# Kernel tuning notes

Measured on AMD Instinct MI355X. Metric: run time of the kernel, lower is better.

Reference implementation:

```python
import jax, jax.numpy as jnp
import numpy as np

N_ATOMS = 500000
MUL0, MUL1, MUL2 = 32, 16, 8      # geometry/output multiplicities for 0e,1o,2e
FMUL0, FMUL1 = 32, 16             # field multiplicities for 0e,1o

# real Wigner 3j for (1,1,2) in e3nn real basis order (l=1: y,z,x ; l=2: xy,yz,z2,zx,x2-y2)
# orthonormal symmetric-traceless basis matrices / sqrt(5) so that sum of squares == 1
def _w3j_112():
    s2 = 1.0 / np.sqrt(2.0); s6 = 1.0 / np.sqrt(6.0)
    C = np.zeros((3, 3, 5), np.float32)
    C[0, 2, 0] = C[2, 0, 0] = s2            # xy
    C[0, 1, 1] = C[1, 0, 1] = s2            # yz
    C[1, 1, 2] = 2.0 * s6; C[0, 0, 2] = -s6; C[2, 2, 2] = -s6  # z2
    C[1, 2, 3] = C[2, 1, 3] = s2            # zx
    C[2, 2, 4] = s2; C[0, 0, 4] = -s2       # x2-y2
    return C / np.sqrt(5.0)

W3J112 = jnp.asarray(_w3j_112())
INV_S3 = float(1.0 / np.sqrt(3.0))   # w3j(0,l,l) = I/sqrt(2l+1), w3j(1,1,0) = I/sqrt(3)
INV_S5 = float(1.0 / np.sqrt(5.0))   # w3j(2,0,2) = I/sqrt(5)
# e3nn FullyConnectedTensorProduct path coefficients (component irrep_normalization, element path_normalization):
# sqrt((2*l_out+1) / sum over paths with same output of mul1*mul2)
C0 = float(np.sqrt(1.0 / (MUL0 * FMUL0 + MUL1 * FMUL1)))          # -> 0e : 1/sqrt(1280)
C1 = float(np.sqrt(3.0 / (MUL0 * FMUL1 + MUL1 * FMUL0 + MUL2 * FMUL1)))  # -> 1o : sqrt(3/1152)
C2 = float(np.sqrt(5.0 / (MUL1 * FMUL1 + MUL2 * FMUL0)))          # -> 2e : sqrt(5/512)


def _forward(geometry_features, field_features,
             w_000, w_011, w_101, w_110, w_112, w_202, w_211,
             wl0, wl1, wl2):
    n = geometry_features.shape[0]
    g0 = geometry_features[:, :32]                       # (n, 32)
    g1 = geometry_features[:, 32:80].reshape(n, 16, 3)   # (n, 16, 3)
    g2 = geometry_features[:, 80:120].reshape(n, 8, 5)   # (n, 8, 5)
    f0 = field_features[:32]                             # (32,)  global, broadcast over atoms
    f1 = field_features[32:].reshape(16, 3)              # (16, 3)

    # --- tensor product paths (uvw connection mode) ---
    out0 = C0 * (jnp.einsum('uvw,zu,v->zw', w_000, g0, f0)
                 + INV_S3 * jnp.einsum('uvw,zui,vi->zw', w_110, g1, f1))
    out1 = C1 * (INV_S3 * jnp.einsum('uvw,zu,vk->zwk', w_011, g0, f1)
                 + INV_S3 * jnp.einsum('uvw,zuk,v->zwk', w_101, g1, f0)
                 + jnp.einsum('uvw,ijk,zuk,vi->zwj', w_211, W3J112, g2, f1))
    out2 = C2 * (jnp.einsum('uvw,ijk,zui,vj->zwk', w_112, W3J112, g1, f1)
                 + INV_S5 * jnp.einsum('uvw,zuk,v->zwk', w_202, g2, f0))

    # --- residual o3.Linear (matching irreps only, 1/sqrt(fan_in)) ---
    r0 = jnp.einsum('uw,zu->zw', wl0, g0) * float(1.0 / np.sqrt(MUL0))
    r1 = jnp.einsum('uw,zui->zwi', wl1, g1) * float(1.0 / np.sqrt(MUL1))
    r2 = jnp.einsum('uw,zui->zwi', wl2, g2) * float(1.0 / np.sqrt(MUL2))

    return jnp.concatenate([out0 + r0,
                            (out1 + r1).reshape(n, 48),
                            (out2 + r2).reshape(n, 40)], axis=1)


def setup_inputs() -> dict:
    key = jax.random.key(0)
    ks = jax.random.split(key, 12)
    rn = lambda k, s: jax.random.normal(k, s, dtype=jnp.float32)
    return {
        'geometry_features': rn(ks[0], (N_ATOMS, 120)),
        'field_features': rn(ks[1], (80,)),
        'w_000': rn(ks[2], (32, 32, 32)),  # (0e,0e)->0e
        'w_011': rn(ks[3], (32, 16, 16)),  # (0e,1o)->1o
        'w_101': rn(ks[4], (16, 32, 16)),  # (1o,0e)->1o
        'w_110': rn(ks[5], (16, 16, 32)),  # (1o,1o)->0e
        'w_112': rn(ks[6], (16, 16, 8)),   # (1o,1o)->2e
        'w_202': rn(ks[7], (8, 32, 8)),    # (2e,0e)->2e
        'w_211': rn(ks[8], (8, 16, 16)),   # (2e,1o)->1o
        'wl0': rn(ks[9], (32, 32)),
        'wl1': rn(ks[10], (16, 16)),
        'wl2': rn(ks[11], (8, 8)),
    }


def reference(geometry_features, field_features,
              w_000, w_011, w_101, w_110, w_112, w_202, w_211,
              wl0, wl1, wl2):
    return _forward(geometry_features, field_features,
                    w_000, w_011, w_101, w_110, w_112, w_202, w_211,
                    wl0, wl1, wl2)
```

## Files before the change

kernel.cpp:

```cpp
#include <hip/hip_runtime.h>

#define LDA 136
#define TM  64

__constant__ float W3J[45] = {
  0.f, 0.f, -0.18257418583505536f, 0.f, -0.31622776601683794f,
  0.f, 0.31622776601683794f, 0.f, 0.f, 0.f,
  0.31622776601683794f, 0.f, 0.f, 0.f, 0.f,
  0.f, 0.31622776601683794f, 0.f, 0.f, 0.f,
  0.f, 0.f, 0.36514837167011072f, 0.f, 0.f,
  0.f, 0.f, 0.f, 0.31622776601683794f, 0.f,
  0.31622776601683794f, 0.f, 0.f, 0.f, 0.f,
  0.f, 0.f, 0.f, 0.31622776601683794f, 0.f,
  0.f, 0.f, -0.18257418583505536f, 0.f, 0.31622776601683794f
};

__device__ __forceinline__ unsigned short f2bf(float f) {
  unsigned int u = __float_as_uint(f);
  u += 0x7FFFu + ((u >> 16) & 1u);
  return (unsigned short)(u >> 16);
}

__global__ void build_B_kernel(
    const float* __restrict__ field,
    const float* __restrict__ w000, const float* __restrict__ w011,
    const float* __restrict__ w101, const float* __restrict__ w110,
    const float* __restrict__ w112, const float* __restrict__ w202,
    const float* __restrict__ w211, const float* __restrict__ wl0,
    const float* __restrict__ wl1,  const float* __restrict__ wl2,
    unsigned short* __restrict__ Bt)
{
  const float C0  = 0.02795084971874737f;
  const float C1  = 0.051031036307982884f;
  const float C2  = 0.09882117688026186f;
  const float IS3 = 0.57735026918962576f;
  const float IS5 = 0.44721359549995794f;

  int n = blockIdx.x;
  int k = threadIdx.x;
  float val = 0.0f;

  if (n < 120 && k < 120) {
    if (n < 32) {
      int w = n;
      if (k < 32) {
        int u = k;
        float a = 0.f;
        for (int v = 0; v < 32; ++v) a += w000[u*1024 + v*32 + w] * field[v];
        val = C0 * a + wl0[u*32 + w] * 0.17677669529663689f;
      } else if (k < 80) {
        int u = (k-32)/3, i = (k-32)%3;
        float a = 0.f;
        for (int v = 0; v < 16; ++v) a += w110[u*512 + v*32 + w] * field[32 + v*3 + i];
        val = C0 * IS3 * a;
      }
    } else if (n < 80) {
      int w = (n-32)/3, j = (n-32)%3;
      if (k < 32) {
        int u = k;
        float a = 0.f;
        for (int v = 0; v < 16; ++v) a += w011[u*256 + v*16 + w] * field[32 + v*3 + j];
        val = C1 * IS3 * a;
      } else if (k < 80) {
        int u = (k-32)/3, i = (k-32)%3;
        if (i == j) {
          float a = 0.f;
          for (int v = 0; v < 32; ++v) a += w101[u*512 + v*16 + w] * field[v];
          val = C1 * IS3 * a + wl1[u*16 + w] * 0.25f;
        }
      } else {
        int u = (k-80)/5, kk = (k-80)%5;
        float c0w = W3J[0*15 + j*5 + kk];
        float c1w = W3J[1*15 + j*5 + kk];
        float c2w = W3J[2*15 + j*5 + kk];
        float a = 0.f;
        for (int v = 0; v < 16; ++v) {
          float s = c0w*field[32+v*3+0] + c1w*field[32+v*3+1] + c2w*field[32+v*3+2];
          a += w211[u*256 + v*16 + w] * s;
        }
        val = C1 * a;
      }
    } else {
      int w = (n-80)/5, k2 = (n-80)%5;
      if (k >= 32 && k < 80) {
        int u = (k-32)/3, i = (k-32)%3;
        float c0w = W3J[i*15 + 0*5 + k2];
        float c1w = W3J[i*15 + 1*5 + k2];
        float c2w = W3J[i*15 + 2*5 + k2];
        float a = 0.f;
        for (int v = 0; v < 16; ++v) {
          float s = c0w*field[32+v*3+0] + c1w*field[32+v*3+1] + c2w*field[32+v*3+2];
          a += w112[u*128 + v*8 + w] * s;
        }
        val = C2 * a;
      } else if (k >= 80) {
        int u = (k-80)/5, kk = (k-80)%5;
        if (kk == k2) {
          float a = 0.f;
          for (int v = 0; v < 32; ++v) a += w202[u*256 + v*8 + w] * field[v];
          val = C2 * IS5 * a + wl2[u*8 + w] * 0.35355339059327378f;
        }
      }
    }
  }
  Bt[n*128 + k] = f2bf(val);
}

typedef __attribute__((ext_vector_type(8))) __bf16 bf16x8;
typedef __attribute__((ext_vector_type(4))) float  f32x4;

__global__ __launch_bounds__(256) void coupling_main(
    const float* __restrict__ geom, const unsigned short* __restrict__ Btg,
    float* __restrict__ out, int natoms)
{
  __shared__ alignas(16) unsigned short Alds[TM  * LDA];
  __shared__ alignas(16) unsigned short Blds[128 * LDA];

  int tid = threadIdx.x;
  long long base = (long long)blockIdx.x * TM;

  #pragma unroll
  for (int r = 0; r < 8; ++r) {
    int g   = tid + r * 256;
    int row = g >> 4;
    int col = (g & 15) * 8;
    uint4 v = ((const uint4*)Btg)[g];
    *((uint4*)&Blds[row * LDA + col]) = v;
  }
  if (tid < TM) {
    *((uint4*)&Alds[tid * LDA + 120]) = make_uint4(0u, 0u, 0u, 0u);
  }
  #pragma unroll
  for (int r = 0; r < 4; ++r) {
    int g = tid + r * 256;
    if (g < 960) {
      int row = g / 15;
      int col = (g - row * 15) * 8;
      long long atom = base + row;
      uint4 pk;
      if (atom < natoms) {
        const float* src = geom + (long long)atom * 120 + col;
        float4 fa = ((const float4*)src)[0];
        float4 fb = ((const float4*)src)[1];
        pk.x = ((unsigned)f2bf(fa.y) << 16) | f2bf(fa.x);
        pk.y = ((unsigned)f2bf(fa.w) << 16) | f2bf(fa.z);
        pk.z = ((unsigned)f2bf(fb.y) << 16) | f2bf(fb.x);
        pk.w = ((unsigned)f2bf(fb.w) << 16) | f2bf(fb.z);
      } else {
        pk = make_uint4(0u, 0u, 0u, 0u);
      }
      *((uint4*)&Alds[row * LDA + col]) = pk;
    }
  }
  __syncthreads();

  int lane = tid & 63;
  int wave = tid >> 6;
  int mrow = lane & 15;
  int kq   = lane >> 4;

  f32x4 zero = {0.f, 0.f, 0.f, 0.f};
  f32x4 acc[8];
  #pragma unroll
  for (int t = 0; t < 8; ++t) acc[t] = zero;

  const unsigned short* arow = &Alds[(wave * 16 + mrow) * LDA + kq * 8];
  const unsigned short* brow = &Blds[mrow * LDA + kq * 8];

  #pragma unroll
  for (int ks = 0; ks < 4; ++ks) {
    bf16x8 af = __builtin_bit_cast(bf16x8, *(const uint4*)(arow + ks * 32));
    #pragma unroll
    for (int t = 0; t < 8; ++t) {
      bf16x8 bf_ = __builtin_bit_cast(bf16x8, *(const uint4*)(brow + t * 16 * LDA + ks * 32));
      acc[t] = __builtin_amdgcn_mfma_f32_16x16x32_bf16(af, bf_, acc[t], 0, 0, 0);
    }
  }

  long long atom0 = base + wave * 16 + kq * 4;
  #pragma unroll
  for (int t = 0; t < 8; ++t) {
    int n = t * 16 + mrow;
    if (n < 120) {
      #pragma unroll
      for (int r2 = 0; r2 < 4; ++r2) {
        long long atom = atom0 + r2;
        if (atom < natoms) out[atom * 120 + n] = acc[t][r2];
      }
    }
  }
}

extern "C" void kernel_launch(void* const* d_in, const int* in_sizes, int n_in,
                              void* d_out, int out_size, void* d_ws, size_t ws_size,
                              hipStream_t stream) {
  const float* geom  = (const float*)d_in[0];
  const float* field = (const float*)d_in[1];
  const float* w000  = (const float*)d_in[2];
  const float* w011  = (const float*)d_in[3];
  const float* w101  = (const float*)d_in[4];
  const float* w110  = (const float*)d_in[5];
  const float* w112  = (const float*)d_in[6];
  const float* w202  = (const float*)d_in[7];
  const float* w211  = (const float*)d_in[8];
  const float* wl0   = (const float*)d_in[9];
  const float* wl1   = (const float*)d_in[10];
  const float* wl2   = (const float*)d_in[11];
  float* out = (float*)d_out;
  unsigned short* Bt = (unsigned short*)d_ws;

  int natoms = in_sizes[0] / 120;

  build_B_kernel<<<dim3(128), dim3(128), 0, stream>>>(
      field, w000, w011, w101, w110, w112, w202, w211, wl0, wl1, wl2, Bt);

  int ntiles = (natoms + TM - 1) / TM;
  coupling_main<<<dim3(ntiles), dim3(256), 0, stream>>>(geom, Bt, out, natoms);
}
```

Measured before the change: 421.7 us.

## Stage output tile through LDS for coalesced nontemporal stores; read B from global

The B matrix is no longer copied into shared memory. Each MFMA now loads its B fragments straight from global memory, where they are expected to hit in cache. The accumulator tile is written to a shared buffer that reuses the A tile's space, then stored to global memory as contiguous float4 rows with nontemporal stores instead of scattered 4-byte writes. This is meant to cut uncoalesced store traffic and shrink the LDS footprint so occupancy can rise. The cost is two extra barriers and B reads going through the cache rather than LDS.

```diff
diff --git a/kernel.cpp b/kernel.cpp
--- a/kernel.cpp
+++ b/kernel.cpp
@@ -2,6 +2,7 @@
 
 #define LDA 136
 #define TM  64
+#define CST 132
 
 __constant__ float W3J[45] = {
   0.f, 0.f, -0.18257418583505536f, 0.f, -0.31622776601683794f,
@@ -113,23 +114,13 @@
     const float* __restrict__ geom, const unsigned short* __restrict__ Btg,
     float* __restrict__ out, int natoms)
 {
-  __shared__ alignas(16) unsigned short Alds[TM  * LDA];
-  __shared__ alignas(16) unsigned short Blds[128 * LDA];
+  __shared__ alignas(16) unsigned char smem[TM * CST * 4];
+  unsigned short* Al = (unsigned short*)smem;
+  float*          Cl = (float*)smem;
 
   int tid = threadIdx.x;
   long long base = (long long)blockIdx.x * TM;
 
-  #pragma unroll
-  for (int r = 0; r < 8; ++r) {
-    int g   = tid + r * 256;
-    int row = g >> 4;
-    int col = (g & 15) * 8;
-    uint4 v = ((const uint4*)Btg)[g];
-    *((uint4*)&Blds[row * LDA + col]) = v;
-  }
-  if (tid < TM) {
-    *((uint4*)&Alds[tid * LDA + 120]) = make_uint4(0u, 0u, 0u, 0u);
-  }
   #pragma unroll
   for (int r = 0; r < 4; ++r) {
     int g = tid + r * 256;
@@ -149,8 +140,11 @@
       } else {
         pk = make_uint4(0u, 0u, 0u, 0u);
       }
-      *((uint4*)&Alds[row * LDA + col]) = pk;
-    }
+      *((uint4*)&Al[row * LDA + col]) = pk;
+    }
+  }
+  if (tid < TM) {
+    *((uint4*)&Al[tid * LDA + 120]) = make_uint4(0u, 0u, 0u, 0u);
   }
   __syncthreads();
 
@@ -164,28 +158,42 @@
   #pragma unroll
   for (int t = 0; t < 8; ++t) acc[t] = zero;
 
-  const unsigned short* arow = &Alds[(wave * 16 + mrow) * LDA + kq * 8];
-  const unsigned short* brow = &Blds[mrow * LDA + kq * 8];
+  const unsigned short* arow = &Al[(wave * 16 + mrow) * LDA + kq * 8];
+  const uint4* Bq = ((const uint4*)Btg) + mrow * 16 + kq;
 
   #pragma unroll
   for (int ks = 0; ks < 4; ++ks) {
     bf16x8 af = __builtin_bit_cast(bf16x8, *(const uint4*)(arow + ks * 32));
     #pragma unroll
     for (int t = 0; t < 8; ++t) {
-      bf16x8 bf_ = __builtin_bit_cast(bf16x8, *(const uint4*)(brow + t * 16 * LDA + ks * 32));
+      bf16x8 bf_ = __builtin_bit_cast(bf16x8, Bq[t * 256 + ks * 4]);
       acc[t] = __builtin_amdgcn_mfma_f32_16x16x32_bf16(af, bf_, acc[t], 0, 0, 0);
     }
   }
 
-  long long atom0 = base + wave * 16 + kq * 4;
+  __syncthreads();
+
+  int crow = wave * 16 + kq * 4;
   #pragma unroll
   for (int t = 0; t < 8; ++t) {
     int n = t * 16 + mrow;
-    if (n < 120) {
-      #pragma unroll
-      for (int r2 = 0; r2 < 4; ++r2) {
-        long long atom = atom0 + r2;
-        if (atom < natoms) out[atom * 120 + n] = acc[t][r2];
+    #pragma unroll
+    for (int r2 = 0; r2 < 4; ++r2) {
+      Cl[(crow + r2) * CST + n] = acc[t][r2];
+    }
+  }
+  __syncthreads();
+
+  #pragma unroll
+  for (int r = 0; r < 8; ++r) {
+    int g = tid + r * 256;
+    if (g < 1920) {
+      int row = g / 30;
+      int c4  = g - row * 30;
+      long long atom = base + row;
+      if (atom < natoms) {
+        f32x4 v = *(const f32x4*)&Cl[row * CST + c4 * 4];
+        __builtin_nontemporal_store(v, (f32x4*)(out + atom * 120 + c4 * 4));
       }
     }
   }
```

Result: slower. 489.2 us (+16.0%).

## Use persistent blocks with register double-buffered prefetch of geometry tiles

Applied to the files above, without the earlier changes.

Launches a capped persistent grid where each block loads the B matrix into LDS once and loops over atom tiles. Geometry rows are loaded straight into registers two tiles ahead, converted to bf16 and fed to MFMA without LDS staging for A. This aims to hide global load latency and remove repeated B loads and per-block sync overhead, at the cost of more registers and less block-level parallelism.

```diff
diff --git a/kernel.cpp b/kernel.cpp
--- a/kernel.cpp
+++ b/kernel.cpp
@@ -109,15 +109,82 @@
 typedef __attribute__((ext_vector_type(8))) __bf16 bf16x8;
 typedef __attribute__((ext_vector_type(4))) float  f32x4;
 
-__global__ __launch_bounds__(256) void coupling_main(
+#define PREFETCH(TT, LO, HI) do {                                        \
+    if ((TT) < ntiles) {                                                 \
+      long long atom_ = (long long)(TT) * TM + rowin;                    \
+      const float* ga_ = geom + atom_ * 120 + kq * 8;                    \
+      bool full_ = ((long long)(TT) * TM + TM) <= (long long)natoms;     \
+      bool ina_  = full_ || (atom_ < natoms);                            \
+      _Pragma("unroll")                                                  \
+      for (int ks_ = 0; ks_ < 4; ++ks_) {                                \
+        bool pad_ = (ks_ == 3) && (kq == 3);                             \
+        if (ina_ && !pad_) {                                             \
+          LO[ks_] = ((const float4*)(ga_ + ks_ * 32))[0];                \
+          HI[ks_] = ((const float4*)(ga_ + ks_ * 32))[1];                \
+        } else { LO[ks_] = f0; HI[ks_] = f0; }                           \
+      }                                                                  \
+    }                                                                    \
+  } while (0)
+
+#define COMPUTE_STORE(TT, LO, HI) do {                                   \
+    bf16x8 af_[4];                                                       \
+    _Pragma("unroll")                                                    \
+    for (int ks_ = 0; ks_ < 4; ++ks_) {                                  \
+      uint4 pk_;                                                         \
+      pk_.x = ((unsigned)f2bf(LO[ks_].y) << 16) | f2bf(LO[ks_].x);       \
+      pk_.y = ((unsigned)f2bf(LO[ks_].w) << 16) | f2bf(LO[ks_].z);       \
+      pk_.z = ((unsigned)f2bf(HI[ks_].y) << 16) | f2bf(HI[ks_].x);       \
+      pk_.w = ((unsigned)f2bf(HI[ks_].w) << 16) | f2bf(HI[ks_].z);       \
+      af_[ks_] = __builtin_bit_cast(bf16x8, pk_);                        \
+    }                                                                    \
+    f32x4 acc_[8];                                                       \
+    _Pragma("unroll")                                                    \
+    for (int t_ = 0; t_ < 8; ++t_) acc_[t_] = (f32x4){0.f,0.f,0.f,0.f};  \
+    _Pragma("unroll")                                                    \
+    for (int ks_ = 0; ks_ < 4; ++ks_) {                                  \
+      _Pragma("unroll")                                                  \
+      for (int t_ = 0; t_ < 8; ++t_) {                                   \
+        bf16x8 bf_ = __builtin_bit_cast(bf16x8,                          \
+            *(const uint4*)(brow + t_ * 16 * LDA + ks_ * 32));           \
+        acc_[t_] = __builtin_amdgcn_mfma_f32_16x16x32_bf16(af_[ks_], bf_, acc_[t_], 0, 0, 0); \
+      }                                                                  \
+    }                                                                    \
+    long long atom0_ = (long long)(TT) * TM + wave * 16 + kq * 4;        \
+    if ((long long)(TT) * TM + TM <= (long long)natoms) {                \
+      _Pragma("unroll")                                                  \
+      for (int t_ = 0; t_ < 8; ++t_) {                                   \
+        int n_ = t_ * 16 + mrow;                                         \
+        if (n_ < 120) {                                                  \
+          _Pragma("unroll")                                              \
+          for (int r_ = 0; r_ < 4; ++r_)                                 \
+            out[(atom0_ + r_) * 120 + n_] = acc_[t_][r_];                \
+        }                                                                \
+      }                                                                  \
+    } else {                                                             \
+      _Pragma("unroll")                                                  \
+      for (int t_ = 0; t_ < 8; ++t_) {                                   \
+        int n_ = t_ * 16 + mrow;                                         \
+        if (n_ < 120) {                                                  \
+          _Pragma("unroll")                                              \
+          for (int r_ = 0; r_ < 4; ++r_)                                 \
+            if (atom0_ + r_ < natoms)                                    \
+              out[(atom0_ + r_) * 120 + n_] = acc_[t_][r_];              \
+        }                                                                \
+      }                                                                  \
+    }                                                                    \
+  } while (0)
+
+__global__ __launch_bounds__(256, 4) void coupling_main(
     const float* __restrict__ geom, const unsigned short* __restrict__ Btg,
-    float* __restrict__ out, int natoms)
+    float* __restrict__ out, int natoms, int ntiles)
 {
-  __shared__ alignas(16) unsigned short Alds[TM  * LDA];
-  __shared__ alignas(16) unsigned short Blds[128 * LDA];
-
-  int tid = threadIdx.x;
-  long long base = (long long)blockIdx.x * TM;
+  __shared__ alignas(16) unsigned short Bl[128 * LDA];
+
+  const int tid  = threadIdx.x;
+  const int lane = tid & 63;
+  const int wave = tid >> 6;
+  const int mrow = lane & 15;
+  const int kq   = lane >> 4;
 
   #pragma unroll
   for (int r = 0; r < 8; ++r) {
@@ -125,69 +192,44 @@
     int row = g >> 4;
     int col = (g & 15) * 8;
     uint4 v = ((const uint4*)Btg)[g];
-    *((uint4*)&Blds[row * LDA + col]) = v;
+    *((uint4*)&Bl[row * LDA + col]) = v;
   }
-  if (tid < TM) {
-    *((uint4*)&Alds[tid * LDA + 120]) = make_uint4(0u, 0u, 0u, 0u);
-  }
-  #pragma unroll
-  for (int r = 0; r < 4; ++r) {
-    int g = tid + r * 256;
-    if (g < 960) {
-      int row = g / 15;
-      int col = (g - row * 15) * 8;
-      long long atom = base + row;
-      uint4 pk;
-      if (atom < natoms) {
-        const float* src = geom + (long long)atom * 120 + col;
-        float4 fa = ((const float4*)src)[0];
-        float4 fb = ((const float4*)src)[1];
-        pk.x = ((unsigned)f2bf(fa.y) << 16) | f2bf(fa.x);
-        pk.y = ((unsigned)f2bf(fa.w) << 16) | f2bf(fa.z);
-        pk.z = ((unsigned)f2bf(fb.y) << 16) | f2bf(fb.x);
-        pk.w = ((unsigned)f2bf(fb.w) << 16) | f2bf(fb.z);
-      } else {
-        pk = make_uint4(0u, 0u, 0u, 0u);
-      }
-      *((uint4*)&Alds[row * LDA + col]) = pk;
+
+  const int rowin = wave * 16 + mrow;
+  const int s = gridDim.x;
+  const float4 f0 = make_float4(0.f, 0.f, 0.f, 0.f);
+
+  float4 p0lo[4], p0hi[4];
+  float4 p1lo[4], p1hi[4];
+
+  int t = blockIdx.x;
+  PREFETCH(t,     p0lo, p0hi);
+  PREFETCH(t + s, p1lo, p1hi);
+
+  __syncthreads();
+
+  const unsigned short* brow = &Bl[mrow * LDA + kq * 8];
+
+  while (true) {
+    if (t >= ntiles) break;
+    {
+      float4 lo[4], hi[4];
+      #pragma unroll
+      for (int i = 0; i < 4; ++i) { lo[i] = p0lo[i]; hi[i] = p0hi[i]; }
+      PREFETCH(t + 2 * s, p0lo, p0hi);
+      COMPUTE_STORE(t, lo, hi);
     }
-  }
-  __syncthreads();
-
-  int lane = tid & 63;
-  int wave = tid >> 6;
-  int mrow = lane & 15;
-  int kq   = lane >> 4;
-
-  f32x4 zero = {0.f, 0.f, 0.f, 0.f};
-  f32x4 acc[8];
-  #pragma unroll
-  for (int t = 0; t < 8; ++t) acc[t] = zero;
-
-  const unsigned short* arow = &Alds[(wave * 16 + mrow) * LDA + kq * 8];
-  const unsigned short* brow = &Blds[mrow * LDA + kq * 8];
-
-  #pragma unroll
-  for (int ks = 0; ks < 4; ++ks) {
-    bf16x8 af = __builtin_bit_cast(bf16x8, *(const uint4*)(arow + ks * 32));
-    #pragma unroll
-    for (int t = 0; t < 8; ++t) {
-      bf16x8 bf_ = __builtin_bit_cast(bf16x8, *(const uint4*)(brow + t * 16 * LDA + ks * 32));
-      acc[t] = __builtin_amdgcn_mfma_f32_16x16x32_bf16(af, bf_, acc[t], 0, 0, 0);
+    t += s;
+
+    if (t >= ntiles) break;
+    {
+      float4 lo[4], hi[4];
+      #pragma unroll
+      for (int i = 0; i < 4; ++i) { lo[i] = p1lo[i]; hi[i] = p1hi[i]; }
+      PREFETCH(t + 2 * s, p1lo, p1hi);
+      COMPUTE_STORE(t, lo, hi);
     }
-  }
-
-  long long atom0 = base + wave * 16 + kq * 4;
-  #pragma unroll
-  for (int t = 0; t < 8; ++t) {
-    int n = t * 16 + mrow;
-    if (n < 120) {
-      #pragma unroll
-      for (int r2 = 0; r2 < 4; ++r2) {
-        long long atom = atom0 + r2;
-        if (atom < natoms) out[atom * 120 + n] = acc[t][r2];
-      }
-    }
+    t += s;
   }
 }
 
@@ -215,5 +257,6 @@
       field, w000, w011, w101, w110, w112, w202, w211, wl0, wl1, wl2, Bt);
 
   int ntiles = (natoms + TM - 1) / TM;
-  coupling_main<<<dim3(ntiles), dim3(256), 0, stream>>>(geom, Bt, out, natoms);
-}
+  int nblk = ntiles < 1024 ? ntiles : 1024;
+  coupling_main<<<dim3(nblk), dim3(256), 0, stream>>>(geom, Bt, out, natoms, ntiles);
+}
```

After: 426.4 us. No clear change (+1.1%).
